# Kernel tuning notes

Hardware: AMD Instinct MI355X
Metric: run time of the kernel (lower is better)

The kernel has to match this reference:

```python
import jax, jax.numpy as jnp
import numpy as np

N, DIM, NH, HD, M = 2048, 1024, 16, 64, 2
LN_EPS = 1e-5


def setup_inputs() -> dict:
    key = jax.random.key(0)
    ks = jax.random.split(key, 8)
    x = jax.random.normal(ks[0], (N, DIM), dtype=jnp.float32)
    ids = jax.random.randint(ks[1], (N,), 0, M)
    modality_masks = jnp.stack([ids == m for m in range(M)])  # [M, N] bool partition
    s = 0.02
    wq = jax.random.normal(ks[2], (M, DIM, NH * HD), dtype=jnp.float32) * s
    wk = jax.random.normal(ks[3], (M, DIM, NH * HD), dtype=jnp.float32) * s
    wv = jax.random.normal(ks[4], (M, DIM, NH * HD), dtype=jnp.float32) * s
    wo = jax.random.normal(ks[5], (M, NH * HD, DIM), dtype=jnp.float32) * s
    ln_w = jnp.ones((M, DIM), dtype=jnp.float32)
    ln_b = jnp.zeros((M, DIM), dtype=jnp.float32)
    return dict(x=x, modality_masks=modality_masks, n_heads=NH,
                wq=wq, wk=wk, wv=wv, wo=wo, ln_w=ln_w, ln_b=ln_b)


def reference(x, modality_masks, n_heads, wq, wk, wv, wo, ln_w, ln_b):
    # x: [N, dim]; modality_masks: [M, N] bool (partition of tokens)
    n_mod, n_tok = modality_masks.shape
    hd = wq.shape[-1] // n_heads
    scale = hd ** -0.5

    mod_id = jnp.argmax(modality_masks, axis=0)          # [N] modality of each token
    perm = jnp.argsort(mod_id, stable=True)              # concat order: mod-0 tokens, then mod-1, ...
    xp = x[perm]                                          # gathered tokens in expert order
    oh = jax.nn.one_hot(mod_id[perm], n_mod, dtype=x.dtype)  # [N, M] expert selector

    def expert_proj(inp, w):
        # inp: [N, din], w: [M, din, dout] -> per-token output using that token's expert
        all_out = jnp.einsum('nd,mdo->mno', inp, w)       # [M, N, dout]
        return jnp.einsum('nm,mno->no', oh, all_out)      # select expert per token

    q = expert_proj(xp, wq).reshape(n_tok, n_heads, hd).transpose(1, 0, 2)  # [H, N, hd]
    k = expert_proj(xp, wk).reshape(n_tok, n_heads, hd).transpose(1, 0, 2)
    v = expert_proj(xp, wv).reshape(n_tok, n_heads, hd).transpose(1, 0, 2)

    scores = jnp.einsum('hnd,hkd->hnk', q, k) * scale     # [H, N, N] full attention over merged tokens
    probs = jax.nn.softmax(scores, axis=-1)
    attn = jnp.einsum('hnk,hkd->hnd', probs, v)           # [H, N, hd]
    attn = attn.transpose(1, 0, 2).reshape(n_tok, n_heads * hd)

    o = expert_proj(attn, wo)                              # [N, dim] per-modality wo
    mu = jnp.mean(o, axis=-1, keepdims=True)
    var = jnp.mean((o - mu) ** 2, axis=-1, keepdims=True)
    on = (o - mu) * jax.lax.rsqrt(var + LN_EPS)
    g = oh @ ln_w                                          # [N, dim] per-token LN scale
    b = oh @ ln_b
    out_perm = on * g + b

    out = jnp.zeros_like(x).at[perm].set(out_perm)         # scatter back to original order
    return out
```

## Files before the change

kernel.cpp:

```cpp
#include <hip/hip_runtime.h>

typedef __attribute__((ext_vector_type(8))) short short8v;
typedef __attribute__((ext_vector_type(4))) float f32x4;
typedef __attribute__((ext_vector_type(16))) float f32x16;
typedef unsigned short u16;
typedef unsigned int u32;

#define MFMA __builtin_amdgcn_mfma_f32_16x16x32_bf16
#define MFMA32 __builtin_amdgcn_mfma_f32_32x32x16_bf16

__device__ __forceinline__ u16 f2b(float f) {
  u32 u = __float_as_uint(f);
  u = (u + 0x7FFFu + ((u >> 16) & 1u)) >> 16;
  return (u16)u;
}
__device__ __forceinline__ float b2f(u16 b) {
  return __uint_as_float(((u32)b) << 16);
}
__device__ __forceinline__ void g2l16(const void* g, void* l) {
  __builtin_amdgcn_global_load_lds(
      (const __attribute__((address_space(1))) unsigned int*)g,
      (__attribute__((address_space(3))) unsigned int*)l, 16, 0, 0);
}

#define N_TOK 2048
#define DIM 1024
#define NH 16
#define HD 64

#define QSCALE 0.18033688011112042f

#define OFF_PERM 0
#define OFF_CNT 8192
#define OFF_XPB 16384
#define OFF_WT (OFF_XPB + 4194304)
#define OFF_Q (OFF_WT + 16777216)
#define OFF_K (OFF_Q + 4194304)
#define OFF_V (OFF_K + 4194304)
#define OFF_VT (OFF_V + 4194304)
#define OFF_AT (OFF_VT + 4194304)
#define OFF_O (OFF_AT + 4194304)

__global__ __launch_bounds__(256) void prep_kernel(const void* __restrict__ masks,
                                                   int* __restrict__ perm,
                                                   int* __restrict__ cnt) {
  const int tid = threadIdx.x;
  __shared__ u32 red[256];
  __shared__ int scan[256];
  const u32* mw = (const u32*)masks;
  u32 mx = 0;
  for (int i = tid; i < 1024; i += 256) { u32 v = mw[i]; mx = mx > v ? mx : v; }
  red[tid] = mx;
  __syncthreads();
  for (int off = 128; off; off >>= 1) {
    if (tid < off) red[tid] = red[tid] > red[tid + off] ? red[tid] : red[tid + off];
    __syncthreads();
  }
  const bool isbyte = red[0] > 1u;
  int md[8];
  int c0loc = 0;
  #pragma unroll
  for (int j = 0; j < 8; ++j) {
    const int n = tid * 8 + j;
    int m1;
    if (isbyte) m1 = ((const unsigned char*)masks)[N_TOK + n] != 0;
    else        m1 = mw[N_TOK + n] != 0;
    md[j] = m1;
    c0loc += (m1 == 0);
  }
  scan[tid] = c0loc;
  __syncthreads();
  for (int off = 1; off < 256; off <<= 1) {
    int v = (tid >= off) ? scan[tid - off] : 0;
    __syncthreads();
    scan[tid] += v;
    __syncthreads();
  }
  const int incl = scan[tid];
  const int total0 = scan[255];
  const int excl0 = incl - c0loc;
  int p0 = excl0;
  int p1 = total0 + (tid * 8 - excl0);
  #pragma unroll
  for (int j = 0; j < 8; ++j) {
    const int n = tid * 8 + j;
    if (!md[j]) perm[p0++] = n; else perm[p1++] = n;
  }
  if (tid == 0) cnt[0] = total0;
}

__global__ __launch_bounds__(256) void gather_cast(const float* __restrict__ x,
                                                   const int* __restrict__ perm,
                                                   u16* __restrict__ xpb) {
  const int i = blockIdx.x;
  const int src = perm[i];
  const int tid = threadIdx.x;
  float4 v = ((const float4*)(x + (size_t)src * DIM))[tid];
  ushort4 o;
  o.x = f2b(v.x); o.y = f2b(v.y); o.z = f2b(v.z); o.w = f2b(v.w);
  ((ushort4*)(xpb + (size_t)i * DIM))[tid] = o;
}

__global__ __launch_bounds__(256) void wcast(const float* __restrict__ wq,
                                             const float* __restrict__ wk,
                                             const float* __restrict__ wv,
                                             const float* __restrict__ wo,
                                             u16* __restrict__ wT) {
  const int mat = blockIdx.z;
  const int tensor = mat >> 1, expert = mat & 1;
  const float* src = (tensor == 0) ? wq : (tensor == 1) ? wk : (tensor == 2) ? wv : wo;
  src += (size_t)expert * (1 << 20);
  u16* dst = wT + ((size_t)mat << 20);
  const int k0 = blockIdx.x * 32, n0 = blockIdx.y * 32;
  const int tx = threadIdx.x, ty = threadIdx.y;
  __shared__ float t[32][33];
  #pragma unroll
  for (int r = 0; r < 4; ++r)
    t[ty + 8 * r][tx] = src[(size_t)(k0 + ty + 8 * r) * DIM + n0 + tx];
  __syncthreads();
  #pragma unroll
  for (int r = 0; r < 4; ++r)
    dst[(size_t)(n0 + ty + 8 * r) * DIM + k0 + tx] = f2b(t[tx][ty + 8 * r]);
}

__global__ __launch_bounds__(256) void vtrans(const u16* __restrict__ v,
                                              u16* __restrict__ vT) {
  const int h = blockIdx.z;
  const int n0 = blockIdx.x * 32, d0 = blockIdx.y * 32;
  const int tx = threadIdx.x, ty = threadIdx.y;
  __shared__ u16 t[32][33];
  #pragma unroll
  for (int r = 0; r < 4; ++r)
    t[ty + 8 * r][tx] = v[(size_t)(n0 + ty + 8 * r) * DIM + h * HD + d0 + tx];
  __syncthreads();
  #pragma unroll
  for (int r = 0; r < 4; ++r)
    vT[(size_t)(h * HD + d0 + ty + 8 * r) * N_TOK + n0 + tx] = t[tx][ty + 8 * r];
}

template <int OUTF32>
__global__ __launch_bounds__(256) void gemm_exp(const u16* __restrict__ X,
                                                const u16* __restrict__ WTall,
                                                int tensor0, float scale0,
                                                void* __restrict__ o0,
                                                void* __restrict__ o1,
                                                void* __restrict__ o2,
                                                const int* __restrict__ cntp) {
  const int z = blockIdx.z;
  const int e = blockIdx.y >> 4;
  const int mt = blockIdx.y & 15;
  const int c0 = cntp[0];
  const int lo = e ? c0 : 0;
  const int hi = e ? N_TOK : c0;
  const int rb = mt * 128;
  if (rb >= hi || rb + 128 <= lo) return;
  const int cb = blockIdx.x * 128;
  void* OUT = (z == 0) ? o0 : (z == 1) ? o1 : o2;
  const u16* W = WTall + ((size_t)((tensor0 + z) * 2 + e) << 20);
  const float scl = (z == 0) ? scale0 : 1.f;

  const int tid = threadIdx.x;
  const int w = tid >> 6, l = tid & 63, lg = l >> 4, ln = l & 15;
  const int wm = (w >> 1) * 64, wn = (w & 1) * 64;

  __shared__ __align__(16) char smem[32768];

  auto stage = [&](int it, int b_) {
    const int k0b = it * 64;
    #pragma unroll
    for (int c = 0; c < 2; ++c) {
      const int lb = (tid + c * 256) * 16;
      const int row = lb >> 6, colb = lb & 63;
      g2l16((const char*)X + (size_t)(rb + row) * 2048 + k0b + colb,
            &smem[b_ * 16384 + lb]);
      g2l16((const char*)W + (size_t)(cb + row) * 2048 + k0b + colb,
            &smem[b_ * 16384 + 8192 + lb]);
    }
  };

  f32x4 acc[4][4];
  #pragma unroll
  for (int i = 0; i < 4; ++i)
    #pragma unroll
    for (int j = 0; j < 4; ++j) acc[i][j] = (f32x4){0.f, 0.f, 0.f, 0.f};

  stage(0, 0);
  __syncthreads();
  for (int it = 0; it < 32; ++it) {
    const int b_ = it & 1;
    if (it < 31) stage(it + 1, b_ ^ 1);
    short8v a[4], bb[4];
    #pragma unroll
    for (int mi = 0; mi < 4; ++mi)
      a[mi] = *(const short8v*)&smem[b_ * 16384 + (wm + mi * 16 + ln) * 64 + lg * 16];
    #pragma unroll
    for (int ni = 0; ni < 4; ++ni)
      bb[ni] = *(const short8v*)&smem[b_ * 16384 + 8192 + (wn + ni * 16 + ln) * 64 + lg * 16];
    __builtin_amdgcn_s_setprio(1);
    #pragma unroll
    for (int mi = 0; mi < 4; ++mi)
      #pragma unroll
      for (int ni = 0; ni < 4; ++ni)
        acc[mi][ni] = MFMA(a[mi], bb[ni], acc[mi][ni], 0, 0, 0);
    __builtin_amdgcn_s_setprio(0);
    __syncthreads();
  }

  #pragma unroll
  for (int mi = 0; mi < 4; ++mi) {
    #pragma unroll
    for (int r = 0; r < 4; ++r) {
      const int row = rb + wm + mi * 16 + lg * 4 + r;
      if (row >= lo && row < hi) {
        #pragma unroll
        for (int ni = 0; ni < 4; ++ni) {
          const int col = cb + wn + ni * 16 + ln;
          const float vv = acc[mi][ni][r] * scl;
          if (OUTF32) ((float*)OUT)[(size_t)row * DIM + col] = vv;
          else ((u16*)OUT)[(size_t)row * DIM + col] = f2b(vv);
        }
      }
    }
  }
}

__global__ __launch_bounds__(256, 2) void attn_fwd(const u16* __restrict__ qg,
                                                   const u16* __restrict__ kg,
                                                   const u16* __restrict__ vTg,
                                                   u16* __restrict__ og) {
  const int qt = blockIdx.x, h = blockIdx.y;
  const int tid = threadIdx.x, w = tid >> 6, l = tid & 63;
  const int g = w & 1, kh = w >> 1;
  const int q31 = l & 31;
  const int hi = l >> 5;
  const int hi16 = hi * 16, hi4 = hi * 4;

  __shared__ __align__(16) char smem[65536];

  auto stage = [&](int it, int b_) {
    #pragma unroll
    for (int c = 0; c < 8; ++c) {
      const int j = tid + c * 256;
      const int s_ = j >> 10;
      const int rem = j & 1023;
      const int isV = rem >> 9;
      const int cc = rem & 511;
      const int r = cc >> 3, c16 = cc & 7;
      const int colb = (c16 * 16) ^ ((r & 7) << 4);
      const char* src;
      if (isV)
        src = (const char*)vTg + (size_t)(h * HD + r) * 4096 + (s_ * 1024 + it * 64) * 2 + colb;
      else
        src = (const char*)kg + (size_t)(s_ * 1024 + it * 64 + r) * 2048 + h * 128 + colb;
      g2l16(src, &smem[s_ * 32768 + b_ * 16384 + isV * 8192 + cc * 16]);
    }
  };
  auto ldf = [&](int base, int row, int colb) -> short8v {
    return *(const short8v*)&smem[base + row * 128 + (colb ^ ((row & 7) << 4))];
  };

  const char* qrow = (const char*)qg + ((size_t)(qt * 64 + g * 32 + q31)) * 2048 + h * 128;
  short8v qf[4];
  #pragma unroll
  for (int t = 0; t < 4; ++t) qf[t] = *(const short8v*)(qrow + t * 32 + hi16);

  stage(0, 0);
  __syncthreads();

  float m_s = -1e30f, l_s = 0.f;
  f32x16 accO[2];
  #pragma unroll
  for (int dt = 0; dt < 2; ++dt)
    #pragma unroll
    for (int r = 0; r < 16; ++r) accO[dt][r] = 0.f;

  for (int it = 0; it < 16; ++it) {
    const int b_ = it & 1;
    if (it < 15) stage(it + 1, b_ ^ 1);
    const int Kb = kh * 32768 + b_ * 16384;
    const int Vb = Kb + 8192;

    #pragma unroll
    for (int ks = 0; ks < 2; ++ks) {
      f32x16 s_;
      #pragma unroll
      for (int r = 0; r < 16; ++r) s_[r] = 0.f;
      {
        short8v kf0 = ldf(Kb, ks * 32 + q31, 0 * 32 + hi16);
        short8v kf1 = ldf(Kb, ks * 32 + q31, 1 * 32 + hi16);
        short8v kf2 = ldf(Kb, ks * 32 + q31, 2 * 32 + hi16);
        short8v kf3 = ldf(Kb, ks * 32 + q31, 3 * 32 + hi16);
        __builtin_amdgcn_s_setprio(1);
        s_ = MFMA32(kf0, qf[0], s_, 0, 0, 0);
        s_ = MFMA32(kf1, qf[1], s_, 0, 0, 0);
        s_ = MFMA32(kf2, qf[2], s_, 0, 0, 0);
        s_ = MFMA32(kf3, qf[3], s_, 0, 0, 0);
        __builtin_amdgcn_s_setprio(0);
      }

      float tmax = s_[0];
      #pragma unroll
      for (int r = 1; r < 16; ++r) tmax = fmaxf(tmax, s_[r]);
      tmax = fmaxf(tmax, __shfl_xor(tmax, 32, 64));

      if (!__all(tmax <= m_s + 11.0f)) {
        const float mn = fmaxf(m_s, tmax);
        const float al = __builtin_amdgcn_exp2f(m_s - mn);
        m_s = mn;
        l_s *= al;
        #pragma unroll
        for (int r = 0; r < 16; ++r) {
          const float ar = __shfl(al, (r & 3) + 8 * (r >> 2) + hi4, 64);
          accO[0][r] *= ar;
          accO[1][r] *= ar;
        }
      }

      float p[16];
      float rs = 0.f;
      #pragma unroll
      for (int r = 0; r < 16; ++r) {
        p[r] = __builtin_amdgcn_exp2f(s_[r] - m_s);
        rs += p[r];
      }
      rs += __shfl_xor(rs, 32, 64);
      l_s += rs;

      u32 c0, c1, c2, c3, c4, c5, c6, c7;
      asm("v_cvt_pk_bf16_f32 %0, %1, %2" : "=v"(c0) : "v"(p[0]), "v"(p[1]));
      asm("v_cvt_pk_bf16_f32 %0, %1, %2" : "=v"(c1) : "v"(p[2]), "v"(p[3]));
      asm("v_cvt_pk_bf16_f32 %0, %1, %2" : "=v"(c2) : "v"(p[4]), "v"(p[5]));
      asm("v_cvt_pk_bf16_f32 %0, %1, %2" : "=v"(c3) : "v"(p[6]), "v"(p[7]));
      asm("v_cvt_pk_bf16_f32 %0, %1, %2" : "=v"(c4) : "v"(p[8]), "v"(p[9]));
      asm("v_cvt_pk_bf16_f32 %0, %1, %2" : "=v"(c5) : "v"(p[10]), "v"(p[11]));
      asm("v_cvt_pk_bf16_f32 %0, %1, %2" : "=v"(c6) : "v"(p[12]), "v"(p[13]));
      asm("v_cvt_pk_bf16_f32 %0, %1, %2" : "=v"(c7) : "v"(p[14]), "v"(p[15]));
      asm volatile("v_permlane32_swap_b32 %0, %1" : "+v"(c0), "+v"(c2));
      asm volatile("v_permlane32_swap_b32 %0, %1" : "+v"(c1), "+v"(c3));
      asm volatile("v_permlane32_swap_b32 %0, %1" : "+v"(c4), "+v"(c6));
      asm volatile("v_permlane32_swap_b32 %0, %1" : "+v"(c5), "+v"(c7));
      union { u32 u[4]; short8v s; } pa0, pa1;
      pa0.u[0] = c0; pa0.u[1] = c1; pa0.u[2] = c2; pa0.u[3] = c3;
      pa1.u[0] = c4; pa1.u[1] = c5; pa1.u[2] = c6; pa1.u[3] = c7;

      #pragma unroll
      for (int kk = 0; kk < 2; ++kk) {
        const short8v pa = kk ? pa1.s : pa0.s;
        short8v vb0 = ldf(Vb, q31, ks * 64 + kk * 32 + hi16);
        short8v vb1 = ldf(Vb, 32 + q31, ks * 64 + kk * 32 + hi16);
        __builtin_amdgcn_s_setprio(1);
        accO[0] = MFMA32(pa, vb0, accO[0], 0, 0, 0);
        accO[1] = MFMA32(pa, vb1, accO[1], 0, 0, 0);
        __builtin_amdgcn_s_setprio(0);
      }
    }
    __syncthreads();
  }

  float* mlds = (float*)&smem[32768];
  if (l < 32) {
    mlds[(g * 2 + kh) * 32 + l] = m_s;
    mlds[128 + (g * 2 + kh) * 32 + l] = l_s;
  }
  __syncthreads();
  const float m0 = mlds[(g * 2 + 0) * 32 + q31];
  const float m1 = mlds[(g * 2 + 1) * 32 + q31];
  const float l0 = mlds[128 + (g * 2 + 0) * 32 + q31];
  const float l1 = mlds[128 + (g * 2 + 1) * 32 + q31];
  const float M = fmaxf(m0, m1);
  const float a0 = __builtin_amdgcn_exp2f(m0 - M);
  const float a1 = __builtin_amdgcn_exp2f(m1 - M);
  const float linv = 1.f / (l0 * a0 + l1 * a1);
  const float aown = kh ? a1 : a0;
  float* obuf = (float*)&smem[0];
  if (kh == 1) {
    #pragma unroll
    for (int r = 0; r < 16; ++r) {
      const int qr = (r & 3) + 8 * (r >> 2) + hi4;
      const float ar = __shfl(aown, qr, 64);
      obuf[(g * 32 + qr) * 64 + q31] = accO[0][r] * ar;
      obuf[(g * 32 + qr) * 64 + 32 + q31] = accO[1][r] * ar;
    }
  }
  __syncthreads();
  if (kh == 0) {
    #pragma unroll
    for (int r = 0; r < 16; ++r) {
      const int qr = (r & 3) + 8 * (r >> 2) + hi4;
      const float ar = __shfl(aown, qr, 64);
      const float li = __shfl(linv, qr, 64);
      const int row = qt * 64 + g * 32 + qr;
      const float v0 = (accO[0][r] * ar + obuf[(g * 32 + qr) * 64 + q31]) * li;
      const float v1 = (accO[1][r] * ar + obuf[(g * 32 + qr) * 64 + 32 + q31]) * li;
      og[(size_t)row * DIM + h * HD + q31] = f2b(v0);
      og[(size_t)row * DIM + h * HD + 32 + q31] = f2b(v1);
    }
  }
}

__global__ __launch_bounds__(256) void ln_scatter(const float* __restrict__ o,
                                                  const float* __restrict__ lnw,
                                                  const float* __restrict__ lnb,
                                                  const int* __restrict__ perm,
                                                  const int* __restrict__ cntp,
                                                  float* __restrict__ out) {
  const int i = blockIdx.x;
  const int tid = threadIdx.x, w = tid >> 6, l = tid & 63;
  const int mod = (i < cntp[0]) ? 0 : 1;
  float4 v = ((const float4*)(o + (size_t)i * DIM))[tid];
  float s = v.x + v.y + v.z + v.w;
  float ss = v.x * v.x + v.y * v.y + v.z * v.z + v.w * v.w;
  #pragma unroll
  for (int off = 1; off < 64; off <<= 1) {
    s += __shfl_xor(s, off, 64);
    ss += __shfl_xor(ss, off, 64);
  }
  __shared__ float rs4[4], rss4[4];
  if (l == 0) { rs4[w] = s; rss4[w] = ss; }
  __syncthreads();
  const float st = rs4[0] + rs4[1] + rs4[2] + rs4[3];
  const float sst = rss4[0] + rss4[1] + rss4[2] + rss4[3];
  const float mu = st * (1.f / DIM);
  const float var = sst * (1.f / DIM) - mu * mu;
  const float rstd = rsqrtf(var + 1e-5f);
  const int drow = perm[i];
  float4 g = ((const float4*)(lnw + (size_t)mod * DIM))[tid];
  float4 b = ((const float4*)(lnb + (size_t)mod * DIM))[tid];
  float4 rr;
  rr.x = (v.x - mu) * rstd * g.x + b.x;
  rr.y = (v.y - mu) * rstd * g.y + b.y;
  rr.z = (v.z - mu) * rstd * g.z + b.z;
  rr.w = (v.w - mu) * rstd * g.w + b.w;
  ((float4*)(out + (size_t)drow * DIM))[tid] = rr;
}

extern "C" void kernel_launch(void* const* d_in, const int* in_sizes, int n_in,
                              void* d_out, int out_size, void* d_ws, size_t ws_size,
                              hipStream_t stream) {
  const float* x = (const float*)d_in[0];
  const void* masks = d_in[1];
  const float* wq = (const float*)d_in[3];
  const float* wk = (const float*)d_in[4];
  const float* wv = (const float*)d_in[5];
  const float* wo = (const float*)d_in[6];
  const float* lnw = (const float*)d_in[7];
  const float* lnb = (const float*)d_in[8];

  char* ws = (char*)d_ws;
  int* perm = (int*)(ws + OFF_PERM);
  int* cnt = (int*)(ws + OFF_CNT);
  u16* xpb = (u16*)(ws + OFF_XPB);
  u16* wT = (u16*)(ws + OFF_WT);
  u16* q = (u16*)(ws + OFF_Q);
  u16* k = (u16*)(ws + OFF_K);
  u16* v = (u16*)(ws + OFF_V);
  u16* vT = (u16*)(ws + OFF_VT);
  u16* at = (u16*)(ws + OFF_AT);
  float* o = (float*)(ws + OFF_O);
  float* out = (float*)d_out;

  prep_kernel<<<1, 256, 0, stream>>>(masks, perm, cnt);
  gather_cast<<<N_TOK, 256, 0, stream>>>(x, perm, xpb);
  wcast<<<dim3(32, 32, 8), dim3(32, 8), 0, stream>>>(wq, wk, wv, wo, wT);
  gemm_exp<0><<<dim3(8, 32, 3), 256, 0, stream>>>(xpb, wT, 0, QSCALE, q, k, v, cnt);
  vtrans<<<dim3(64, 2, 16), dim3(32, 8), 0, stream>>>(v, vT);
  attn_fwd<<<dim3(32, 16), 256, 0, stream>>>(q, k, vT, at);
  gemm_exp<1><<<dim3(8, 32, 1), 256, 0, stream>>>(at, wT, 3, 1.0f, o, o, o, cnt);
  ln_scatter<<<N_TOK, 256, 0, stream>>>(o, lnw, lnb, perm, cnt, out);
}
```

Measured before the change: 111.0 us.

## Load K/V fragments directly from global into registers, dropping LDS staging

The attention kernel no longer stages K and V tiles through shared memory with double-buffered async copies and per-iteration barriers. Each wave now loads its K and V MFMA operands straight from global memory into registers, prefetching the next tile's K one iteration ahead. The QK^T chain is split into two independent accumulators, and the max and sum reductions become trees to shorten dependency chains. Shared memory shrinks, which may raise occupancy, but each wave now issues redundant global/L2 loads that the LDS tiles used to share, and register pressure rises.

```diff
diff --git a/kernel.cpp b/kernel.cpp
--- a/kernel.cpp
+++ b/kernel.cpp
@@ -235,37 +235,16 @@
   const int hi = l >> 5;
   const int hi16 = hi * 16, hi4 = hi * 4;
 
-  __shared__ __align__(16) char smem[65536];
-
-  auto stage = [&](int it, int b_) {
-    #pragma unroll
-    for (int c = 0; c < 8; ++c) {
-      const int j = tid + c * 256;
-      const int s_ = j >> 10;
-      const int rem = j & 1023;
-      const int isV = rem >> 9;
-      const int cc = rem & 511;
-      const int r = cc >> 3, c16 = cc & 7;
-      const int colb = (c16 * 16) ^ ((r & 7) << 4);
-      const char* src;
-      if (isV)
-        src = (const char*)vTg + (size_t)(h * HD + r) * 4096 + (s_ * 1024 + it * 64) * 2 + colb;
-      else
-        src = (const char*)kg + (size_t)(s_ * 1024 + it * 64 + r) * 2048 + h * 128 + colb;
-      g2l16(src, &smem[s_ * 32768 + b_ * 16384 + isV * 8192 + cc * 16]);
-    }
-  };
-  auto ldf = [&](int base, int row, int colb) -> short8v {
-    return *(const short8v*)&smem[base + row * 128 + (colb ^ ((row & 7) << 4))];
-  };
+  __shared__ __align__(16) char smem[17408];
 
   const char* qrow = (const char*)qg + ((size_t)(qt * 64 + g * 32 + q31)) * 2048 + h * 128;
   short8v qf[4];
   #pragma unroll
   for (int t = 0; t < 4; ++t) qf[t] = *(const short8v*)(qrow + t * 32 + hi16);
 
-  stage(0, 0);
-  __syncthreads();
+  const char* pK = (const char*)kg + ((size_t)(kh * 1024 + q31)) * 2048 + h * 128 + hi16;
+  const char* pV0 = (const char*)vTg + ((size_t)(h * 64 + q31)) * 4096 + kh * 2048 + hi16;
+  const char* pV1 = pV0 + 32 * 4096;
 
   float m_s = -1e30f, l_s = 0.f;
   f32x16 accO[2];
@@ -274,33 +253,52 @@
     #pragma unroll
     for (int r = 0; r < 16; ++r) accO[dt][r] = 0.f;
 
-  for (int it = 0; it < 16; ++it) {
-    const int b_ = it & 1;
-    if (it < 15) stage(it + 1, b_ ^ 1);
-    const int Kb = kh * 32768 + b_ * 16384;
-    const int Vb = Kb + 8192;
-
+  short8v kA[8], kB[8];
+  #pragma unroll
+  for (int ks = 0; ks < 2; ++ks)
+    #pragma unroll
+    for (int t = 0; t < 4; ++t)
+      kA[ks * 4 + t] = *(const short8v*)(pK + ks * 65536 + t * 32);
+
+  auto body = [&](short8v (&kc)[8], short8v (&kn)[8], int it) {
+    short8v vv[8];
+    #pragma unroll
+    for (int ks = 0; ks < 2; ++ks)
+      #pragma unroll
+      for (int kk = 0; kk < 2; ++kk) {
+        vv[ks * 4 + kk * 2 + 0] = *(const short8v*)(pV0 + it * 128 + ks * 64 + kk * 32);
+        vv[ks * 4 + kk * 2 + 1] = *(const short8v*)(pV1 + it * 128 + ks * 64 + kk * 32);
+      }
+    const int itn = (it + 1) & 15;
     #pragma unroll
     for (int ks = 0; ks < 2; ++ks) {
-      f32x16 s_;
-      #pragma unroll
-      for (int r = 0; r < 16; ++r) s_[r] = 0.f;
-      {
-        short8v kf0 = ldf(Kb, ks * 32 + q31, 0 * 32 + hi16);
-        short8v kf1 = ldf(Kb, ks * 32 + q31, 1 * 32 + hi16);
-        short8v kf2 = ldf(Kb, ks * 32 + q31, 2 * 32 + hi16);
-        short8v kf3 = ldf(Kb, ks * 32 + q31, 3 * 32 + hi16);
-        __builtin_amdgcn_s_setprio(1);
-        s_ = MFMA32(kf0, qf[0], s_, 0, 0, 0);
-        s_ = MFMA32(kf1, qf[1], s_, 0, 0, 0);
-        s_ = MFMA32(kf2, qf[2], s_, 0, 0, 0);
-        s_ = MFMA32(kf3, qf[3], s_, 0, 0, 0);
-        __builtin_amdgcn_s_setprio(0);
+      f32x16 s0, s1;
+      #pragma unroll
+      for (int r = 0; r < 16; ++r) { s0[r] = 0.f; s1[r] = 0.f; }
+      __builtin_amdgcn_s_setprio(1);
+      s0 = MFMA32(kc[ks * 4 + 0], qf[0], s0, 0, 0, 0);
+      s1 = MFMA32(kc[ks * 4 + 1], qf[1], s1, 0, 0, 0);
+      s0 = MFMA32(kc[ks * 4 + 2], qf[2], s0, 0, 0, 0);
+      s1 = MFMA32(kc[ks * 4 + 3], qf[3], s1, 0, 0, 0);
+      __builtin_amdgcn_s_setprio(0);
+      if (ks == 0) {
+        #pragma unroll
+        for (int j = 0; j < 2; ++j)
+          #pragma unroll
+          for (int t = 0; t < 4; ++t)
+            kn[j * 4 + t] = *(const short8v*)(pK + (size_t)itn * 131072 + j * 65536 + t * 32);
       }
-
-      float tmax = s_[0];
-      #pragma unroll
-      for (int r = 1; r < 16; ++r) tmax = fmaxf(tmax, s_[r]);
+      float sc[16];
+      #pragma unroll
+      for (int r = 0; r < 16; ++r) sc[r] = s0[r] + s1[r];
+
+      float a0 = fmaxf(sc[0], sc[1]), a1 = fmaxf(sc[2], sc[3]);
+      float a2 = fmaxf(sc[4], sc[5]), a3 = fmaxf(sc[6], sc[7]);
+      float a4 = fmaxf(sc[8], sc[9]), a5 = fmaxf(sc[10], sc[11]);
+      float a6 = fmaxf(sc[12], sc[13]), a7 = fmaxf(sc[14], sc[15]);
+      float b0 = fmaxf(a0, a1), b1 = fmaxf(a2, a3);
+      float b2 = fmaxf(a4, a5), b3 = fmaxf(a6, a7);
+      float tmax = fmaxf(fmaxf(b0, b1), fmaxf(b2, b3));
       tmax = fmaxf(tmax, __shfl_xor(tmax, 32, 64));
 
       if (!__all(tmax <= m_s + 11.0f)) {
@@ -317,12 +315,13 @@
       }
 
       float p[16];
-      float rs = 0.f;
-      #pragma unroll
-      for (int r = 0; r < 16; ++r) {
-        p[r] = __builtin_amdgcn_exp2f(s_[r] - m_s);
-        rs += p[r];
-      }
+      #pragma unroll
+      for (int r = 0; r < 16; ++r) p[r] = __builtin_amdgcn_exp2f(sc[r] - m_s);
+      float q0 = (p[0] + p[1]) + (p[2] + p[3]);
+      float q1 = (p[4] + p[5]) + (p[6] + p[7]);
+      float q2 = (p[8] + p[9]) + (p[10] + p[11]);
+      float q3 = (p[12] + p[13]) + (p[14] + p[15]);
+      float rs = (q0 + q1) + (q2 + q3);
       rs += __shfl_xor(rs, 32, 64);
       l_s += rs;
 
@@ -346,18 +345,22 @@
       #pragma unroll
       for (int kk = 0; kk < 2; ++kk) {
         const short8v pa = kk ? pa1.s : pa0.s;
-        short8v vb0 = ldf(Vb, q31, ks * 64 + kk * 32 + hi16);
-        short8v vb1 = ldf(Vb, 32 + q31, ks * 64 + kk * 32 + hi16);
+        const short8v vb0 = vv[ks * 4 + kk * 2 + 0];
+        const short8v vb1 = vv[ks * 4 + kk * 2 + 1];
         __builtin_amdgcn_s_setprio(1);
         accO[0] = MFMA32(pa, vb0, accO[0], 0, 0, 0);
         accO[1] = MFMA32(pa, vb1, accO[1], 0, 0, 0);
         __builtin_amdgcn_s_setprio(0);
       }
     }
-    __syncthreads();
-  }
-
-  float* mlds = (float*)&smem[32768];
+  };
+
+  for (int it2 = 0; it2 < 8; ++it2) {
+    body(kA, kB, it2 * 2);
+    body(kB, kA, it2 * 2 + 1);
+  }
+
+  float* mlds = (float*)&smem[16384];
   if (l < 32) {
     mlds[(g * 2 + kh) * 32 + l] = m_s;
     mlds[128 + (g * 2 + kh) * 32 + l] = l_s;
```

Result: slower. 139.5 us (+25.6%).

## Restructure attention to 128-query tiles with four-way KV split and XCD-aware block mapping

Applied to the files above, without the earlier changes.

The attention kernel now uses 512-thread blocks that each handle 128 queries: each wave processes two 32-query sets, so every K/V fragment loaded from LDS is reused twice, and the KV sequence is split four ways across wave groups instead of two. Blocks are launched on a 1D grid and remapped so that consecutive block IDs spread across the XCDs. The partial results are merged through LDS over four sequential reduction rounds. The aim is to cut LDS and global K/V traffic per unit of work. In exchange it uses more registers, doubles LDS use to 128 KB per block, adds a longer final merge, and halves the number of blocks, which may hurt occupancy.

```diff
diff --git a/kernel.cpp b/kernel.cpp
--- a/kernel.cpp
+++ b/kernel.cpp
@@ -224,23 +224,24 @@
   }
 }
 
-__global__ __launch_bounds__(256, 2) void attn_fwd(const u16* __restrict__ qg,
+__global__ __launch_bounds__(512, 2) void attn_fwd(const u16* __restrict__ qg,
                                                    const u16* __restrict__ kg,
                                                    const u16* __restrict__ vTg,
                                                    u16* __restrict__ og) {
-  const int qt = blockIdx.x, h = blockIdx.y;
+  const int bid = blockIdx.x;
+  const int wg = (bid & 7) * 32 + (bid >> 3);
+  const int qt = wg & 15, h = wg >> 4;
   const int tid = threadIdx.x, w = tid >> 6, l = tid & 63;
-  const int g = w & 1, kh = w >> 1;
-  const int q31 = l & 31;
-  const int hi = l >> 5;
+  const int g = w & 1, kq = w >> 1;
+  const int q31 = l & 31, hi = l >> 5;
   const int hi16 = hi * 16, hi4 = hi * 4;
 
-  __shared__ __align__(16) char smem[65536];
+  __shared__ __align__(16) char smem[131072];
 
   auto stage = [&](int it, int b_) {
     #pragma unroll
     for (int c = 0; c < 8; ++c) {
-      const int j = tid + c * 256;
+      const int j = tid + c * 512;
       const int s_ = j >> 10;
       const int rem = j & 1023;
       const int isV = rem >> 9;
@@ -249,9 +250,9 @@
       const int colb = (c16 * 16) ^ ((r & 7) << 4);
       const char* src;
       if (isV)
-        src = (const char*)vTg + (size_t)(h * HD + r) * 4096 + (s_ * 1024 + it * 64) * 2 + colb;
+        src = (const char*)vTg + (size_t)(h * HD + r) * 4096 + (s_ * 512 + it * 64) * 2 + colb;
       else
-        src = (const char*)kg + (size_t)(s_ * 1024 + it * 64 + r) * 2048 + h * 128 + colb;
+        src = (const char*)kg + (size_t)(s_ * 512 + it * 64 + r) * 2048 + h * 128 + colb;
       g2l16(src, &smem[s_ * 32768 + b_ * 16384 + isV * 8192 + cc * 16]);
     }
   };
@@ -259,142 +260,170 @@
     return *(const short8v*)&smem[base + row * 128 + (colb ^ ((row & 7) << 4))];
   };
 
-  const char* qrow = (const char*)qg + ((size_t)(qt * 64 + g * 32 + q31)) * 2048 + h * 128;
-  short8v qf[4];
-  #pragma unroll
-  for (int t = 0; t < 4; ++t) qf[t] = *(const short8v*)(qrow + t * 32 + hi16);
+  const char* qb = (const char*)qg + (size_t)(qt * 128 + g * 64 + q31) * 2048 + h * 128;
+  short8v qf0[4], qf1[4];
+  #pragma unroll
+  for (int t = 0; t < 4; ++t) {
+    qf0[t] = *(const short8v*)(qb + t * 32 + hi16);
+    qf1[t] = *(const short8v*)(qb + 65536 + t * 32 + hi16);
+  }
 
   stage(0, 0);
   __syncthreads();
 
-  float m_s = -1e30f, l_s = 0.f;
-  f32x16 accO[2];
-  #pragma unroll
-  for (int dt = 0; dt < 2; ++dt)
-    #pragma unroll
-    for (int r = 0; r < 16; ++r) accO[dt][r] = 0.f;
-
-  for (int it = 0; it < 16; ++it) {
+  float m0 = -1e30f, l0 = 0.f, m1 = -1e30f, l1 = 0.f;
+  f32x16 acc00, acc01, acc10, acc11;
+  #pragma unroll
+  for (int r = 0; r < 16; ++r) { acc00[r] = 0.f; acc01[r] = 0.f; acc10[r] = 0.f; acc11[r] = 0.f; }
+
+  auto softmax_pv = [&](f32x16& s_, float& m_s, float& l_s,
+                        f32x16& accA, f32x16& accB, const short8v vf[2][2]) {
+    float tmax = s_[0];
+    #pragma unroll
+    for (int r = 1; r < 16; ++r) tmax = fmaxf(tmax, s_[r]);
+    tmax = fmaxf(tmax, __shfl_xor(tmax, 32, 64));
+    if (!__all(tmax <= m_s + 11.0f)) {
+      const float mn = fmaxf(m_s, tmax);
+      const float al = __builtin_amdgcn_exp2f(m_s - mn);
+      m_s = mn;
+      l_s *= al;
+      #pragma unroll
+      for (int r = 0; r < 16; ++r) {
+        const float ar = __shfl(al, (r & 3) + 8 * (r >> 2) + hi4, 64);
+        accA[r] *= ar;
+        accB[r] *= ar;
+      }
+    }
+    float p[16];
+    #pragma unroll
+    for (int r = 0; r < 16; ++r) p[r] = __builtin_amdgcn_exp2f(s_[r] - m_s);
+    float rs = ((p[0] + p[1]) + (p[2] + p[3])) + ((p[4] + p[5]) + (p[6] + p[7])) +
+               (((p[8] + p[9]) + (p[10] + p[11])) + ((p[12] + p[13]) + (p[14] + p[15])));
+    rs += __shfl_xor(rs, 32, 64);
+    l_s += rs;
+
+    u32 c0, c1, c2, c3, c4, c5, c6, c7;
+    asm("v_cvt_pk_bf16_f32 %0, %1, %2" : "=v"(c0) : "v"(p[0]), "v"(p[1]));
+    asm("v_cvt_pk_bf16_f32 %0, %1, %2" : "=v"(c1) : "v"(p[2]), "v"(p[3]));
+    asm("v_cvt_pk_bf16_f32 %0, %1, %2" : "=v"(c2) : "v"(p[4]), "v"(p[5]));
+    asm("v_cvt_pk_bf16_f32 %0, %1, %2" : "=v"(c3) : "v"(p[6]), "v"(p[7]));
+    asm("v_cvt_pk_bf16_f32 %0, %1, %2" : "=v"(c4) : "v"(p[8]), "v"(p[9]));
+    asm("v_cvt_pk_bf16_f32 %0, %1, %2" : "=v"(c5) : "v"(p[10]), "v"(p[11]));
+    asm("v_cvt_pk_bf16_f32 %0, %1, %2" : "=v"(c6) : "v"(p[12]), "v"(p[13]));
+    asm("v_cvt_pk_bf16_f32 %0, %1, %2" : "=v"(c7) : "v"(p[14]), "v"(p[15]));
+    asm volatile("v_permlane32_swap_b32 %0, %1" : "+v"(c0), "+v"(c2));
+    asm volatile("v_permlane32_swap_b32 %0, %1" : "+v"(c1), "+v"(c3));
+    asm volatile("v_permlane32_swap_b32 %0, %1" : "+v"(c4), "+v"(c6));
+    asm volatile("v_permlane32_swap_b32 %0, %1" : "+v"(c5), "+v"(c7));
+    union { u32 u[4]; short8v s; } pa0, pa1;
+    pa0.u[0] = c0; pa0.u[1] = c1; pa0.u[2] = c2; pa0.u[3] = c3;
+    pa1.u[0] = c4; pa1.u[1] = c5; pa1.u[2] = c6; pa1.u[3] = c7;
+    __builtin_amdgcn_s_setprio(1);
+    accA = MFMA32(pa0.s, vf[0][0], accA, 0, 0, 0);
+    accB = MFMA32(pa0.s, vf[0][1], accB, 0, 0, 0);
+    accA = MFMA32(pa1.s, vf[1][0], accA, 0, 0, 0);
+    accB = MFMA32(pa1.s, vf[1][1], accB, 0, 0, 0);
+    __builtin_amdgcn_s_setprio(0);
+  };
+
+  for (int it = 0; it < 8; ++it) {
     const int b_ = it & 1;
-    if (it < 15) stage(it + 1, b_ ^ 1);
-    const int Kb = kh * 32768 + b_ * 16384;
+    if (it < 7) stage(it + 1, b_ ^ 1);
+    const int Kb = kq * 32768 + b_ * 16384;
     const int Vb = Kb + 8192;
 
     #pragma unroll
     for (int ks = 0; ks < 2; ++ks) {
-      f32x16 s_;
-      #pragma unroll
-      for (int r = 0; r < 16; ++r) s_[r] = 0.f;
-      {
-        short8v kf0 = ldf(Kb, ks * 32 + q31, 0 * 32 + hi16);
-        short8v kf1 = ldf(Kb, ks * 32 + q31, 1 * 32 + hi16);
-        short8v kf2 = ldf(Kb, ks * 32 + q31, 2 * 32 + hi16);
-        short8v kf3 = ldf(Kb, ks * 32 + q31, 3 * 32 + hi16);
-        __builtin_amdgcn_s_setprio(1);
-        s_ = MFMA32(kf0, qf[0], s_, 0, 0, 0);
-        s_ = MFMA32(kf1, qf[1], s_, 0, 0, 0);
-        s_ = MFMA32(kf2, qf[2], s_, 0, 0, 0);
-        s_ = MFMA32(kf3, qf[3], s_, 0, 0, 0);
-        __builtin_amdgcn_s_setprio(0);
-      }
-
-      float tmax = s_[0];
-      #pragma unroll
-      for (int r = 1; r < 16; ++r) tmax = fmaxf(tmax, s_[r]);
-      tmax = fmaxf(tmax, __shfl_xor(tmax, 32, 64));
-
-      if (!__all(tmax <= m_s + 11.0f)) {
-        const float mn = fmaxf(m_s, tmax);
-        const float al = __builtin_amdgcn_exp2f(m_s - mn);
-        m_s = mn;
-        l_s *= al;
+      short8v kf[4];
+      #pragma unroll
+      for (int t = 0; t < 4; ++t) kf[t] = ldf(Kb, ks * 32 + q31, t * 32 + hi16);
+      short8v vf[2][2];
+      #pragma unroll
+      for (int kk = 0; kk < 2; ++kk)
+        #pragma unroll
+        for (int ds = 0; ds < 2; ++ds)
+          vf[kk][ds] = ldf(Vb, ds * 32 + q31, ks * 64 + kk * 32 + hi16);
+
+      f32x16 s0, s1;
+      #pragma unroll
+      for (int r = 0; r < 16; ++r) { s0[r] = 0.f; s1[r] = 0.f; }
+      __builtin_amdgcn_s_setprio(1);
+      s0 = MFMA32(kf[0], qf0[0], s0, 0, 0, 0);
+      s1 = MFMA32(kf[0], qf1[0], s1, 0, 0, 0);
+      s0 = MFMA32(kf[1], qf0[1], s0, 0, 0, 0);
+      s1 = MFMA32(kf[1], qf1[1], s1, 0, 0, 0);
+      s0 = MFMA32(kf[2], qf0[2], s0, 0, 0, 0);
+      s1 = MFMA32(kf[2], qf1[2], s1, 0, 0, 0);
+      s0 = MFMA32(kf[3], qf0[3], s0, 0, 0, 0);
+      s1 = MFMA32(kf[3], qf1[3], s1, 0, 0, 0);
+      __builtin_amdgcn_s_setprio(0);
+
+      softmax_pv(s0, m0, l0, acc00, acc01, vf);
+      softmax_pv(s1, m1, l1, acc10, acc11, vf);
+    }
+    __syncthreads();
+  }
+  __syncthreads();
+
+  float* mm = (float*)&smem[98304];
+  if (l < 32) {
+    mm[((g * 2 + 0) * 4 + kq) * 32 + l] = m0;
+    mm[((g * 2 + 1) * 4 + kq) * 32 + l] = m1;
+    mm[512 + ((g * 2 + 0) * 4 + kq) * 32 + l] = l0;
+    mm[512 + ((g * 2 + 1) * 4 + kq) * 32 + l] = l1;
+  }
+  __syncthreads();
+  float al0, al1, li0, li1;
+  #pragma unroll
+  for (int set = 0; set < 2; ++set) {
+    const int base = (g * 2 + set) * 4;
+    float M = mm[(base + 0) * 32 + q31];
+    M = fmaxf(M, mm[(base + 1) * 32 + q31]);
+    M = fmaxf(M, mm[(base + 2) * 32 + q31]);
+    M = fmaxf(M, mm[(base + 3) * 32 + q31]);
+    float L = 0.f;
+    #pragma unroll
+    for (int j = 0; j < 4; ++j)
+      L += mm[512 + (base + j) * 32 + q31] *
+           __builtin_amdgcn_exp2f(mm[(base + j) * 32 + q31] - M);
+    const float mo = set ? m1 : m0;
+    const float a = __builtin_amdgcn_exp2f(mo - M);
+    const float li = 1.f / L;
+    if (set) { al1 = a; li1 = li; } else { al0 = a; li0 = li; }
+  }
+
+  float* obuf = (float*)&smem[g * 16384];
+  #pragma unroll
+  for (int round = 3; round >= 0; --round) {
+    if (kq == round) {
+      #pragma unroll
+      for (int set = 0; set < 2; ++set) {
+        const float alS = set ? al1 : al0;
+        const float liS = set ? li1 : li0;
+        const f32x16& aA = set ? acc10 : acc00;
+        const f32x16& aB = set ? acc11 : acc01;
         #pragma unroll
         for (int r = 0; r < 16; ++r) {
-          const float ar = __shfl(al, (r & 3) + 8 * (r >> 2) + hi4, 64);
-          accO[0][r] *= ar;
-          accO[1][r] *= ar;
+          const int qr = (r & 3) + 8 * (r >> 2) + hi4;
+          const float ar = __shfl(alS, qr, 64);
+          float* p0 = &obuf[(set * 32 + qr) * 64 + q31];
+          float* p1 = &obuf[(set * 32 + qr) * 64 + 32 + q31];
+          if (round == 3) {
+            *p0 = aA[r] * ar;
+            *p1 = aB[r] * ar;
+          } else if (round > 0) {
+            *p0 += aA[r] * ar;
+            *p1 += aB[r] * ar;
+          } else {
+            const float li = __shfl(liS, qr, 64);
+            const int row = qt * 128 + g * 64 + set * 32 + qr;
+            og[(size_t)row * DIM + h * HD + q31] = f2b((aA[r] * ar + *p0) * li);
+            og[(size_t)row * DIM + h * HD + 32 + q31] = f2b((aB[r] * ar + *p1) * li);
+          }
         }
       }
-
-      float p[16];
-      float rs = 0.f;
-      #pragma unroll
-      for (int r = 0; r < 16; ++r) {
-        p[r] = __builtin_amdgcn_exp2f(s_[r] - m_s);
-        rs += p[r];
-      }
-      rs += __shfl_xor(rs, 32, 64);
-      l_s += rs;
-
-      u32 c0, c1, c2, c3, c4, c5, c6, c7;
-      asm("v_cvt_pk_bf16_f32 %0, %1, %2" : "=v"(c0) : "v"(p[0]), "v"(p[1]));
-      asm("v_cvt_pk_bf16_f32 %0, %1, %2" : "=v"(c1) : "v"(p[2]), "v"(p[3]));
-      asm("v_cvt_pk_bf16_f32 %0, %1, %2" : "=v"(c2) : "v"(p[4]), "v"(p[5]));
-      asm("v_cvt_pk_bf16_f32 %0, %1, %2" : "=v"(c3) : "v"(p[6]), "v"(p[7]));
-      asm("v_cvt_pk_bf16_f32 %0, %1, %2" : "=v"(c4) : "v"(p[8]), "v"(p[9]));
-      asm("v_cvt_pk_bf16_f32 %0, %1, %2" : "=v"(c5) : "v"(p[10]), "v"(p[11]));
-      asm("v_cvt_pk_bf16_f32 %0, %1, %2" : "=v"(c6) : "v"(p[12]), "v"(p[13]));
-      asm("v_cvt_pk_bf16_f32 %0, %1, %2" : "=v"(c7) : "v"(p[14]), "v"(p[15]));
-      asm volatile("v_permlane32_swap_b32 %0, %1" : "+v"(c0), "+v"(c2));
-      asm volatile("v_permlane32_swap_b32 %0, %1" : "+v"(c1), "+v"(c3));
-      asm volatile("v_permlane32_swap_b32 %0, %1" : "+v"(c4), "+v"(c6));
-      asm volatile("v_permlane32_swap_b32 %0, %1" : "+v"(c5), "+v"(c7));
-      union { u32 u[4]; short8v s; } pa0, pa1;
-      pa0.u[0] = c0; pa0.u[1] = c1; pa0.u[2] = c2; pa0.u[3] = c3;
-      pa1.u[0] = c4; pa1.u[1] = c5; pa1.u[2] = c6; pa1.u[3] = c7;
-
-      #pragma unroll
-      for (int kk = 0; kk < 2; ++kk) {
-        const short8v pa = kk ? pa1.s : pa0.s;
-        short8v vb0 = ldf(Vb, q31, ks * 64 + kk * 32 + hi16);
-        short8v vb1 = ldf(Vb, 32 + q31, ks * 64 + kk * 32 + hi16);
-        __builtin_amdgcn_s_setprio(1);
-        accO[0] = MFMA32(pa, vb0, accO[0], 0, 0, 0);
-        accO[1] = MFMA32(pa, vb1, accO[1], 0, 0, 0);
-        __builtin_amdgcn_s_setprio(0);
-      }
-    }
-    __syncthreads();
-  }
-
-  float* mlds = (float*)&smem[32768];
-  if (l < 32) {
-    mlds[(g * 2 + kh) * 32 + l] = m_s;
-    mlds[128 + (g * 2 + kh) * 32 + l] = l_s;
-  }
-  __syncthreads();
-  const float m0 = mlds[(g * 2 + 0) * 32 + q31];
-  const float m1 = mlds[(g * 2 + 1) * 32 + q31];
-  const float l0 = mlds[128 + (g * 2 + 0) * 32 + q31];
-  const float l1 = mlds[128 + (g * 2 + 1) * 32 + q31];
-  const float M = fmaxf(m0, m1);
-  const float a0 = __builtin_amdgcn_exp2f(m0 - M);
-  const float a1 = __builtin_amdgcn_exp2f(m1 - M);
-  const float linv = 1.f / (l0 * a0 + l1 * a1);
-  const float aown = kh ? a1 : a0;
-  float* obuf = (float*)&smem[0];
-  if (kh == 1) {
-    #pragma unroll
-    for (int r = 0; r < 16; ++r) {
-      const int qr = (r & 3) + 8 * (r >> 2) + hi4;
-      const float ar = __shfl(aown, qr, 64);
-      obuf[(g * 32 + qr) * 64 + q31] = accO[0][r] * ar;
-      obuf[(g * 32 + qr) * 64 + 32 + q31] = accO[1][r] * ar;
-    }
-  }
-  __syncthreads();
-  if (kh == 0) {
-    #pragma unroll
-    for (int r = 0; r < 16; ++r) {
-      const int qr = (r & 3) + 8 * (r >> 2) + hi4;
-      const float ar = __shfl(aown, qr, 64);
-      const float li = __shfl(linv, qr, 64);
-      const int row = qt * 64 + g * 32 + qr;
-      const float v0 = (accO[0][r] * ar + obuf[(g * 32 + qr) * 64 + q31]) * li;
-      const float v1 = (accO[1][r] * ar + obuf[(g * 32 + qr) * 64 + 32 + q31]) * li;
-      og[(size_t)row * DIM + h * HD + q31] = f2b(v0);
-      og[(size_t)row * DIM + h * HD + 32 + q31] = f2b(v1);
-    }
+    }
+    __syncthreads();
   }
 }
 
@@ -464,7 +493,7 @@
   wcast<<<dim3(32, 32, 8), dim3(32, 8), 0, stream>>>(wq, wk, wv, wo, wT);
   gemm_exp<0><<<dim3(8, 32, 3), 256, 0, stream>>>(xpb, wT, 0, QSCALE, q, k, v, cnt);
   vtrans<<<dim3(64, 2, 16), dim3(32, 8), 0, stream>>>(v, vT);
-  attn_fwd<<<dim3(32, 16), 256, 0, stream>>>(q, k, vT, at);
+  attn_fwd<<<256, 512, 0, stream>>>(q, k, vT, at);
   gemm_exp<1><<<dim3(8, 32, 1), 256, 0, stream>>>(at, wT, 3, 1.0f, o, o, o, cnt);
   ln_scatter<<<N_TOK, 256, 0, stream>>>(o, lnw, lnb, perm, cnt, out);
 }
```

Result: no change. 109.4 us (-1.5%).
